# Optimization experiments

Measured on AMD Instinct MI355X. Metric: run time of the kernel, lower is better.

The kernel has to match this reference:

```python
import jax, jax.numpy as jnp
import numpy as np

IN_F = 256
OUT_F = 256
ALPHA = 0.2  # LeakyReLU negative slope


def _xavier(key, shape, gain=1.414):
    fan_in, fan_out = shape[0], shape[1]
    limit = gain * np.sqrt(6.0 / (fan_in + fan_out))
    return jax.random.uniform(key, shape, jnp.float32, -limit, limit)


def setup_inputs() -> dict:
    key = jax.random.key(0)
    k1, k2, k3, k4, k5, k6 = jax.random.split(key, 6)
    B, N = 8, 2048
    h = jax.random.normal(k1, (B, N, IN_F), jnp.float32)
    adj = jax.random.randint(k2, (B, N, N), 0, 2, jnp.int32)
    lrgt1 = jax.random.normal(k3, (B, N, OUT_F), jnp.float32)
    W1 = _xavier(k4, (IN_F, IN_F))
    W2 = _xavier(k5, (OUT_F, OUT_F))
    a = _xavier(k6, (2 * IN_F, 1))
    return {"h": h, "adj": adj, "lrgt1": lrgt1, "W1": W1, "W2": W2, "a": a}


def reference(h, adj, lrgt1, W1, W2, a):
    # Wh: [B,N,in], wlrgt: [B,N,out]
    Wh = jnp.matmul(h, W1)
    wlrgt = jnp.matmul(lrgt1, W2)
    # additive attention scores: e[b,i,j] = leaky_relu(Wh_i @ a1 + Wh_j @ a2)
    a1 = a[:IN_F, 0]   # [in]
    a2 = a[IN_F:, 0]   # [in]
    Wh1 = jnp.einsum('bnc,c->bn', Wh, a1)  # [B,N]
    Wh2 = jnp.einsum('bnc,c->bn', Wh, a2)  # [B,N]
    e = jax.nn.leaky_relu(Wh1[:, :, None] + Wh2[:, None, :], ALPHA)  # [B,N,N]
    neg = jnp.float32(-9e15)
    masked = jnp.where(adj > 0, e, neg)
    attention = jax.nn.softmax(masked, axis=2)
    # dropout p=0.0 / eval mode -> identity
    h_prime = jnp.matmul(attention, Wh)      # [B,N,in]
    gt_prime = jnp.matmul(attention, wlrgt)  # [B,N,out]
    return (jax.nn.elu(h_prime), jax.nn.elu(gt_prime))
```

## Files before the change

kernel.cpp:

```cpp
#include <hip/hip_runtime.h>
#include <hip/hip_bf16.h>

#define IN_F 256
#define NN   2048
#define BB   8

typedef unsigned short u16;
typedef __attribute__((ext_vector_type(8))) short short8x;
typedef __attribute__((ext_vector_type(4))) float float4x;

__device__ __forceinline__ u16 f2b(float f) {
    union { float f; unsigned int u; } x; x.f = f;
    unsigned int r = x.u + 0x7FFFu + ((x.u >> 16) & 1u);
    return (u16)(r >> 16);
}

__device__ __forceinline__ void transp_body(const float* __restrict__ src,
                                            u16* __restrict__ dst,
                                            int R, int C, int tid,
                                            float (*tile)[33])
{
    const int per = (R / 32) * (C / 32);
    const int b  = tid / per;
    const int tt = tid % per;
    const int jt = tt / (C / 32);
    const int ct = tt % (C / 32);
    src += (long)b * R * C;
    dst += (long)b * R * C;

    const int tx = threadIdx.x & 31, ty = threadIdx.x >> 5;
#pragma unroll
    for (int i = 0; i < 4; ++i)
        tile[ty + i * 8][tx] = src[(long)(jt * 32 + ty + i * 8) * C + ct * 32 + tx];
    __syncthreads();
#pragma unroll
    for (int i = 0; i < 4; ++i)
        dst[(long)(ct * 32 + ty + i * 8) * R + jt * 32 + tx] = f2b(tile[tx][ty + i * 8]);
}

__global__ __launch_bounds__(256) void prep(const float* __restrict__ h,
                                            const float* __restrict__ g,
                                            const float* __restrict__ W1,
                                            const float* __restrict__ W2,
                                            const float* __restrict__ a,
                                            u16* __restrict__ HbfT,
                                            u16* __restrict__ GbfT,
                                            u16* __restrict__ W1T,
                                            u16* __restrict__ W2T,
                                            float* __restrict__ v1,
                                            float* __restrict__ v2)
{
    __shared__ float tile[32][33];
    __shared__ float s1[IN_F], s2[IN_F];
    const int bid = blockIdx.x;

    if (bid < 4096) {
        transp_body(h, HbfT, NN, IN_F, bid, tile);
    } else if (bid < 8192) {
        transp_body(g, GbfT, NN, IN_F, bid - 4096, tile);
    } else if (bid < 8256) {
        transp_body(W1, W1T, IN_F, IN_F, bid - 8192, tile);
    } else if (bid < 8320) {
        transp_body(W2, W2T, IN_F, IN_F, bid - 8256, tile);
    } else {
        const int t = threadIdx.x;
        s1[t] = a[t];
        s2[t] = a[IN_F + t];
        __syncthreads();
        float acc1 = 0.f, acc2 = 0.f;
        for (int c = 0; c < IN_F; ++c) {
            float w = W1[t * IN_F + c];
            acc1 += w * s1[c];
            acc2 += w * s2[c];
        }
        v1[t] = acc1;
        v2[t] = acc2;
    }
}

__global__ __launch_bounds__(256) void rowdots(const float* __restrict__ h,
                                               const float* __restrict__ v1,
                                               const float* __restrict__ v2,
                                               float* __restrict__ Wh1,
                                               float* __restrict__ Wh2)
{
    const int wave = threadIdx.x >> 6;
    const int lane = threadIdx.x & 63;
    const long row = (long)blockIdx.x * 4 + wave;
    const int c0 = lane * 4;

    float4 v  = *(const float4*)(h + row * IN_F + c0);
    float4 a1 = *(const float4*)(v1 + c0);
    float4 a2 = *(const float4*)(v2 + c0);

    float s1 = v.x * a1.x + v.y * a1.y + v.z * a1.z + v.w * a1.w;
    float s2 = v.x * a2.x + v.y * a2.y + v.z * a2.z + v.w * a2.w;
#pragma unroll
    for (int off = 32; off; off >>= 1) {
        s1 += __shfl_xor(s1, off, 64);
        s2 += __shfl_xor(s2, off, 64);
    }
    if (lane == 0) { Wh1[row] = s1; Wh2[row] = s2; }
}

#define KSTEP(ksv, BC, BN_, AC, AN_, do_a, jnxt)                              \
    {                                                                         \
        if (do_a) {                                                           \
            _Pragma("unroll") for (int rt = 0; rt < 4; ++rt)                  \
                AN_[rt] = *(const short8x*)&ab[(((ksv) + 1) * 4 + rt) * 512 + lane * 8]; \
        }                                                                     \
        _Pragma("unroll") for (int ct = 0; ct < 4; ++ct)                      \
            BN_[ct] = *(const short8x*)(Bp + ct * 16 * NN + (jnxt));          \
        _Pragma("unroll") for (int rt = 0; rt < 4; ++rt)                      \
            _Pragma("unroll") for (int ct = 0; ct < 4; ++ct)                  \
                acc[rt][ct] = __builtin_amdgcn_mfma_f32_16x16x32_bf16(AC[rt], BC[ct], acc[rt][ct], 0, 0, 0); \
    }

#define CHUNK7(KCH, ADJC, ADJN)                                               \
    {                                                                         \
        const int j0 = (KCH) * 128;                                           \
        union { short8x v; u16 e[8]; } pk0, pk1, pk2, pk3;                    \
        _Pragma("unroll") for (int u = 0; u < 8; ++u) {                       \
            const float4 wv = *(const float4*)&wh2L[j0 + sg * 32 + u * 4];    \
            const float wf[4] = {wv.x, wv.y, wv.z, wv.w};                     \
            const int   av[4] = {ADJC[u].x, ADJC[u].y, ADJC[u].z, ADJC[u].w}; \
            _Pragma("unroll") for (int c = 0; c < 4; ++c) {                   \
                float x = wh1rr + wf[c];                                      \
                float ev = fmaxf(x, 0.2f * x);                                \
                float p = __expf(ev - mv);                                    \
                p = (av[c] > 0) ? p : 0.0f;                                   \
                lloc += p;                                                    \
                u16 fv = f2b(p);                                              \
                if (u < 2)      pk0.e[(u & 1) * 4 + c] = fv;                  \
                else if (u < 4) pk1.e[(u & 1) * 4 + c] = fv;                  \
                else if (u < 6) pk2.e[(u & 1) * 4 + c] = fv;                  \
                else            pk3.e[(u & 1) * 4 + c] = fv;                  \
            }                                                                 \
        }                                                                     \
        if ((KCH) < 15) {                                                     \
            const long o = adjR + ((KCH) + 1) * 128 + sg * 32;                \
            _Pragma("unroll") for (int u = 0; u < 8; ++u)                     \
                ADJN[u] = *(const int4*)(adj + o + u * 4);                    \
        }                                                                     \
        u16* ab = &Afrag[(KCH) & 1][0];                                       \
        *(short8x*)&ab[wbase0]       = pk0.v;                                 \
        *(short8x*)&ab[wbase0 + 128] = pk1.v;                                 \
        *(short8x*)&ab[wbase0 + 256] = pk2.v;                                 \
        *(short8x*)&ab[wbase0 + 384] = pk3.v;                                 \
        asm volatile("s_waitcnt lgkmcnt(0)\n\ts_barrier" ::: "memory");       \
        _Pragma("unroll") for (int rt = 0; rt < 4; ++rt)                      \
            A0[rt] = *(const short8x*)&ab[rt * 512 + lane * 8];               \
        KSTEP(0, B0, B1, A0, A1, 1, j0 + 1 * 32 + bq8)                        \
        KSTEP(1, B1, B0, A1, A0, 1, j0 + 2 * 32 + bq8)                        \
        KSTEP(2, B0, B1, A0, A1, 1, j0 + 3 * 32 + bq8)                        \
        KSTEP(3, B1, B0, A1, A0, 0, (((KCH) < 15) ? (j0 + 128) : j0) + bq8)   \
    }

__global__ __launch_bounds__(256, 2) void attn_mfma(
    const int* __restrict__ adj,
    const u16* __restrict__ HbfT, const u16* __restrict__ GbfT,
    const float* __restrict__ Wh1, const float* __restrict__ Wh2,
    u16* __restrict__ PH, u16* __restrict__ PG)
{
    const int t = threadIdx.x;
    const int wave = t >> 6, lane = t & 63;
    const int b   = blockIdx.x & 7;
    const int idx = blockIdx.x >> 3;
    const int mat = idx & 1;
    const int rbl = idx >> 1;
    const long gi0 = ((long)b * 32 + rbl) * 64;

    __shared__ __align__(16) u16 Afrag[2][8192];
    __shared__ float wh2L[2048];
    __shared__ float sred[256];
    __shared__ float ssc[65];

    const int rr = t >> 2, sg = t & 3;
    const long adjR = (gi0 + rr) * (long)NN;
    const float* wh2b = Wh2 + (long)b * NN;
    const float wh1rr = Wh1[gi0 + rr];

    {
        float4 w0 = *(const float4*)(wh2b + t * 8);
        float4 w1 = *(const float4*)(wh2b + t * 8 + 4);
        *(float4*)&wh2L[t * 8]     = w0;
        *(float4*)&wh2L[t * 8 + 4] = w1;
        float m = fmaxf(fmaxf(fmaxf(w0.x, w0.y), fmaxf(w0.z, w0.w)),
                        fmaxf(fmaxf(w1.x, w1.y), fmaxf(w1.z, w1.w)));
        sred[t] = m;
    }
    __syncthreads();
    if (t < 64) {
        float v = fmaxf(fmaxf(sred[t * 4], sred[t * 4 + 1]),
                        fmaxf(sred[t * 4 + 2], sred[t * 4 + 3]));
#pragma unroll
        for (int off = 32; off; off >>= 1) v = fmaxf(v, __shfl_xor(v, off, 64));
        if (t == 0) ssc[64] = v;
    }
    __syncthreads();
    const float mm = wh1rr + ssc[64];
    const float mv = (mm >= 0.f) ? mm : 0.2f * mm;

    const int wbase0 = (sg * 4 + (rr >> 4)) * 512 + (rr & 15) * 8;

    float4x acc[4][4];
#pragma unroll
    for (int rt = 0; rt < 4; ++rt)
#pragma unroll
        for (int ct = 0; ct < 4; ++ct) acc[rt][ct] = (float4x)0.0f;

    const int bn = lane & 15, bq = lane >> 4, bq8 = bq * 8;
    const u16* Bp = (mat ? GbfT : HbfT) + (long)b * IN_F * NN
                  + (long)(wave * 64 + bn) * NN;

    float lloc = 0.f;

    short8x A0[4], A1[4], B0[4], B1[4];
    int4 adjA[8], adjB[8];

#pragma unroll
    for (int u = 0; u < 8; ++u)
        adjA[u] = *(const int4*)(adj + adjR + sg * 32 + u * 4);
#pragma unroll
    for (int u = 0; u < 8; ++u)
        adjB[u] = *(const int4*)(adj + adjR + 128 + sg * 32 + u * 4);
#pragma unroll
    for (int ct = 0; ct < 4; ++ct)
        B0[ct] = *(const short8x*)(Bp + ct * 16 * NN + bq8);

    for (int kp = 0; kp < 8; ++kp) {
        CHUNK7(kp * 2,     adjA, adjB)
        CHUNK7(kp * 2 + 1, adjB, adjA)
    }

    sred[t] = lloc;
    __syncthreads();
    if (t < 64) {
        float v = sred[t * 4] + sred[t * 4 + 1] + sred[t * 4 + 2] + sred[t * 4 + 3];
        ssc[t] = 1.0f / v;
    }
    __syncthreads();

    u16* dst = mat ? PG : PH;
    const int colb = wave * 64;
#pragma unroll
    for (int rt = 0; rt < 4; ++rt)
#pragma unroll
        for (int ct = 0; ct < 4; ++ct) {
            const int c = colb + ct * 16 + bn;
#pragma unroll
            for (int reg = 0; reg < 4; ++reg) {
                const int rl = rt * 16 + bq * 4 + reg;
                const float il = ssc[rl];
                const long row = gi0 + rl;
                dst[row * IN_F + c] = f2b(acc[rt][ct][reg] * il);
            }
        }
}

__global__ __launch_bounds__(256) void epi2(const u16* __restrict__ PH,
                                            const u16* __restrict__ PG,
                                            const u16* __restrict__ W1T,
                                            const u16* __restrict__ W2T,
                                            float* __restrict__ out)
{
    int bid = blockIdx.x;
    const u16* X;
    const u16* WT;
    float* o;
    if (bid < 512) { X = PH; WT = W1T; o = out; }
    else           { X = PG; WT = W2T; o = out + (long)BB * NN * IN_F; bid -= 512; }

    const int t = threadIdx.x;
    const int wave = t >> 6, lane = t & 63;
    const long i0 = (long)bid * 32;

    __shared__ __align__(16) u16 Afrag[8 * 2 * 64 * 8];

    const int m = t >> 3, ks0 = t & 7, rt0 = m >> 4, lm = m & 15;
    const u16* xp = X + (i0 + m) * IN_F + ks0 * 32;
#pragma unroll
    for (int q = 0; q < 4; ++q) {
        short8x v = *(const short8x*)(xp + q * 8);
        *(short8x*)&Afrag[((ks0 * 2 + rt0) * 64 + lm + q * 16) * 8] = v;
    }
    __syncthreads();

    float4x acc[2][4];
#pragma unroll
    for (int rt = 0; rt < 2; ++rt)
#pragma unroll
        for (int ct = 0; ct < 4; ++ct) acc[rt][ct] = (float4x)0.0f;

    const int bn = lane & 15, bq = lane >> 4;
#pragma unroll
    for (int ks = 0; ks < 8; ++ks) {
        short8x A0 = *(const short8x*)&Afrag[((ks * 2 + 0) * 64 + lane) * 8];
        short8x A1 = *(const short8x*)&Afrag[((ks * 2 + 1) * 64 + lane) * 8];
#pragma unroll
        for (int ct = 0; ct < 4; ++ct) {
            const int n = wave * 64 + ct * 16 + bn;
            short8x Bw = *(const short8x*)(WT + n * IN_F + ks * 32 + bq * 8);
            acc[0][ct] = __builtin_amdgcn_mfma_f32_16x16x32_bf16(A0, Bw, acc[0][ct], 0, 0, 0);
            acc[1][ct] = __builtin_amdgcn_mfma_f32_16x16x32_bf16(A1, Bw, acc[1][ct], 0, 0, 0);
        }
    }

#pragma unroll
    for (int rt = 0; rt < 2; ++rt)
#pragma unroll
        for (int ct = 0; ct < 4; ++ct) {
            const int n = wave * 64 + ct * 16 + bn;
#pragma unroll
            for (int reg = 0; reg < 4; ++reg) {
                const long row = i0 + rt * 16 + bq * 4 + reg;
                float v = acc[rt][ct][reg];
                v = (v > 0.f) ? v : (__expf(v) - 1.f);
                o[row * IN_F + n] = v;
            }
        }
}

extern "C" void kernel_launch(void* const* d_in, const int* in_sizes, int n_in,
                              void* d_out, int out_size, void* d_ws, size_t ws_size,
                              hipStream_t stream)
{
    int ih = -1, ig = -1, iadj = -1, iw1 = -1, iw2 = -1, ia = -1;
    for (int i = 0; i < n_in; ++i) {
        int s = in_sizes[i];
        if      (s == BB * NN * NN)   { if (iadj < 0) iadj = i; }
        else if (s == BB * NN * IN_F) { if (ih < 0) ih = i; else if (ig < 0) ig = i; }
        else if (s == IN_F * IN_F)    { if (iw1 < 0) iw1 = i; else if (iw2 < 0) iw2 = i; }
        else if (s == 2 * IN_F)       { if (ia < 0) ia = i; }
    }
    if (ih < 0 || ig < 0 || iadj < 0 || iw1 < 0 || iw2 < 0 || ia < 0) {
        ih = 0; iadj = 1; ig = 2; iw1 = 3; iw2 = 4; ia = 5;
    }
    const float* h     = (const float*)d_in[ih];
    const int*   adj   = (const int*)  d_in[iadj];
    const float* lrgt1 = (const float*)d_in[ig];
    const float* W1    = (const float*)d_in[iw1];
    const float* W2    = (const float*)d_in[iw2];
    const float* a     = (const float*)d_in[ia];
    float* out = (float*)d_out;

    float* ws   = (float*)d_ws;
    float* v1   = ws;
    float* v2   = v1 + IN_F;
    float* Wh1  = v2 + IN_F;
    float* Wh2  = Wh1 + BB * NN;
    u16* W1T  = (u16*)(Wh2 + BB * NN);
    u16* W2T  = W1T + IN_F * IN_F;
    u16* HbfT = W2T + IN_F * IN_F;
    u16* GbfT = HbfT + (long)BB * IN_F * NN;
    u16* PH   = GbfT + (long)BB * IN_F * NN;
    u16* PG   = PH + (long)BB * NN * IN_F;

    const int nrows = BB * NN;

    prep     <<<8321,        256, 0, stream>>>(h, lrgt1, W1, W2, a,
                                               HbfT, GbfT, W1T, W2T, v1, v2);
    rowdots  <<<nrows / 4,   256, 0, stream>>>(h, v1, v2, Wh1, Wh2);
    attn_mfma<<<nrows / 32,  256, 0, stream>>>(adj, HbfT, GbfT, Wh1, Wh2, PH, PG);
    epi2     <<<2 * nrows / 32, 256, 0, stream>>>(PH, PG, W1T, W2T, out);
}
```

Baseline: 324.1 us.

## Halve attention row tile to 32 rows, bit-pack adjacency mask, vectorize transpose

The attention kernel now processes 32 query rows per block instead of 64, with 8 threads per row and half the accumulator tiles, so register and LDS use drop and launch bounds rise to 4 blocks per SM. The grid doubles. Adjacency values for the next chunk are loaded as four int4 values and packed into a 16-bit mask, which replaces holding 16 int4 registers. The prep transpose now uses float4 loads and ushort4 stores. The aim is higher occupancy and fewer registers, at the cost of rereading the B (HbfT/GbfT) operand twice as often across blocks.

```diff
diff --git a/kernel.cpp b/kernel.cpp
--- a/kernel.cpp
+++ b/kernel.cpp
@@ -15,10 +15,10 @@
     return (u16)(r >> 16);
 }
 
-__device__ __forceinline__ void transp_body(const float* __restrict__ src,
-                                            u16* __restrict__ dst,
-                                            int R, int C, int tid,
-                                            float (*tile)[33])
+__device__ __forceinline__ void transp_body4(const float* __restrict__ src,
+                                             u16* __restrict__ dst,
+                                             int R, int C, int tid,
+                                             float (*tile)[33])
 {
     const int per = (R / 32) * (C / 32);
     const int b  = tid / per;
@@ -28,14 +28,21 @@
     src += (long)b * R * C;
     dst += (long)b * R * C;
 
-    const int tx = threadIdx.x & 31, ty = threadIdx.x >> 5;
-#pragma unroll
-    for (int i = 0; i < 4; ++i)
-        tile[ty + i * 8][tx] = src[(long)(jt * 32 + ty + i * 8) * C + ct * 32 + tx];
-    __syncthreads();
-#pragma unroll
-    for (int i = 0; i < 4; ++i)
-        dst[(long)(ct * 32 + ty + i * 8) * R + jt * 32 + tx] = f2b(tile[tx][ty + i * 8]);
+    const int t = threadIdx.x;
+    const int lr = t >> 3, lc = (t & 7) * 4;
+    float4 v = *(const float4*)(src + (long)(jt * 32 + lr) * C + ct * 32 + lc);
+    tile[lr][lc + 0] = v.x;
+    tile[lr][lc + 1] = v.y;
+    tile[lr][lc + 2] = v.z;
+    tile[lr][lc + 3] = v.w;
+    __syncthreads();
+    const int c = t >> 3, r4 = (t & 7) * 4;
+    ushort4 o;
+    o.x = f2b(tile[r4 + 0][c]);
+    o.y = f2b(tile[r4 + 1][c]);
+    o.z = f2b(tile[r4 + 2][c]);
+    o.w = f2b(tile[r4 + 3][c]);
+    *(ushort4*)(dst + (long)(ct * 32 + c) * R + jt * 32 + r4) = o;
 }
 
 __global__ __launch_bounds__(256) void prep(const float* __restrict__ h,
@@ -55,13 +62,13 @@
     const int bid = blockIdx.x;
 
     if (bid < 4096) {
-        transp_body(h, HbfT, NN, IN_F, bid, tile);
+        transp_body4(h, HbfT, NN, IN_F, bid, tile);
     } else if (bid < 8192) {
-        transp_body(g, GbfT, NN, IN_F, bid - 4096, tile);
+        transp_body4(g, GbfT, NN, IN_F, bid - 4096, tile);
     } else if (bid < 8256) {
-        transp_body(W1, W1T, IN_F, IN_F, bid - 8192, tile);
+        transp_body4(W1, W1T, IN_F, IN_F, bid - 8192, tile);
     } else if (bid < 8320) {
-        transp_body(W2, W2T, IN_F, IN_F, bid - 8256, tile);
+        transp_body4(W2, W2T, IN_F, IN_F, bid - 8256, tile);
     } else {
         const int t = threadIdx.x;
         s1[t] = a[t];
@@ -103,60 +110,63 @@
     if (lane == 0) { Wh1[row] = s1; Wh2[row] = s2; }
 }
 
-#define KSTEP(ksv, BC, BN_, AC, AN_, do_a, jnxt)                              \
+#define KS8(KSV, BC, BN_, jnxt)                                               \
     {                                                                         \
-        if (do_a) {                                                           \
-            _Pragma("unroll") for (int rt = 0; rt < 4; ++rt)                  \
-                AN_[rt] = *(const short8x*)&ab[(((ksv) + 1) * 4 + rt) * 512 + lane * 8]; \
-        }                                                                     \
+        short8x Ar0 = *(const short8x*)&ab[(((KSV) * 2 + 0) * 64 + lane) * 8];\
+        short8x Ar1 = *(const short8x*)&ab[(((KSV) * 2 + 1) * 64 + lane) * 8];\
         _Pragma("unroll") for (int ct = 0; ct < 4; ++ct)                      \
             BN_[ct] = *(const short8x*)(Bp + ct * 16 * NN + (jnxt));          \
-        _Pragma("unroll") for (int rt = 0; rt < 4; ++rt)                      \
-            _Pragma("unroll") for (int ct = 0; ct < 4; ++ct)                  \
-                acc[rt][ct] = __builtin_amdgcn_mfma_f32_16x16x32_bf16(AC[rt], BC[ct], acc[rt][ct], 0, 0, 0); \
-    }
-
-#define CHUNK7(KCH, ADJC, ADJN)                                               \
+        _Pragma("unroll") for (int ct = 0; ct < 4; ++ct) {                    \
+            acc[0][ct] = __builtin_amdgcn_mfma_f32_16x16x32_bf16(Ar0, BC[ct], acc[0][ct], 0, 0, 0); \
+            acc[1][ct] = __builtin_amdgcn_mfma_f32_16x16x32_bf16(Ar1, BC[ct], acc[1][ct], 0, 0, 0); \
+        }                                                                     \
+    }
+
+#define PK4(I4, BASE)                                                         \
+    pb |= ((unsigned)(I4.x > 0) << (BASE))     | ((unsigned)(I4.y > 0) << ((BASE)+1)) | \
+          ((unsigned)(I4.z > 0) << ((BASE)+2)) | ((unsigned)(I4.w > 0) << ((BASE)+3));
+
+#define CHUNK8(KCH)                                                           \
     {                                                                         \
         const int j0 = (KCH) * 128;                                           \
-        union { short8x v; u16 e[8]; } pk0, pk1, pk2, pk3;                    \
-        _Pragma("unroll") for (int u = 0; u < 8; ++u) {                       \
-            const float4 wv = *(const float4*)&wh2L[j0 + sg * 32 + u * 4];    \
+        union { short8x v; u16 e[8]; } pk0, pk1;                              \
+        _Pragma("unroll") for (int u = 0; u < 4; ++u) {                       \
+            const float4 wv = *(const float4*)&wh2L[j0 + sg * 16 + u * 4];    \
             const float wf[4] = {wv.x, wv.y, wv.z, wv.w};                     \
-            const int   av[4] = {ADJC[u].x, ADJC[u].y, ADJC[u].z, ADJC[u].w}; \
             _Pragma("unroll") for (int c = 0; c < 4; ++c) {                   \
                 float x = wh1rr + wf[c];                                      \
                 float ev = fmaxf(x, 0.2f * x);                                \
                 float p = __expf(ev - mv);                                    \
-                p = (av[c] > 0) ? p : 0.0f;                                   \
+                p = ((mk >> (u * 4 + c)) & 1u) ? p : 0.0f;                    \
                 lloc += p;                                                    \
                 u16 fv = f2b(p);                                              \
-                if (u < 2)      pk0.e[(u & 1) * 4 + c] = fv;                  \
-                else if (u < 4) pk1.e[(u & 1) * 4 + c] = fv;                  \
-                else if (u < 6) pk2.e[(u & 1) * 4 + c] = fv;                  \
-                else            pk3.e[(u & 1) * 4 + c] = fv;                  \
+                if (u < 2) pk0.e[u * 4 + c] = fv;                             \
+                else       pk1.e[(u - 2) * 4 + c] = fv;                       \
             }                                                                 \
         }                                                                     \
         if ((KCH) < 15) {                                                     \
-            const long o = adjR + ((KCH) + 1) * 128 + sg * 32;                \
-            _Pragma("unroll") for (int u = 0; u < 8; ++u)                     \
-                ADJN[u] = *(const int4*)(adj + o + u * 4);                    \
+            const long o = adjR + ((KCH) + 1) * 128 + sg * 16;                \
+            i0 = *(const int4*)(adj + o);                                     \
+            i1 = *(const int4*)(adj + o + 4);                                 \
+            i2 = *(const int4*)(adj + o + 8);                                 \
+            i3 = *(const int4*)(adj + o + 12);                                \
         }                                                                     \
         u16* ab = &Afrag[(KCH) & 1][0];                                       \
         *(short8x*)&ab[wbase0]       = pk0.v;                                 \
         *(short8x*)&ab[wbase0 + 128] = pk1.v;                                 \
-        *(short8x*)&ab[wbase0 + 256] = pk2.v;                                 \
-        *(short8x*)&ab[wbase0 + 384] = pk3.v;                                 \
         asm volatile("s_waitcnt lgkmcnt(0)\n\ts_barrier" ::: "memory");       \
-        _Pragma("unroll") for (int rt = 0; rt < 4; ++rt)                      \
-            A0[rt] = *(const short8x*)&ab[rt * 512 + lane * 8];               \
-        KSTEP(0, B0, B1, A0, A1, 1, j0 + 1 * 32 + bq8)                        \
-        KSTEP(1, B1, B0, A1, A0, 1, j0 + 2 * 32 + bq8)                        \
-        KSTEP(2, B0, B1, A0, A1, 1, j0 + 3 * 32 + bq8)                        \
-        KSTEP(3, B1, B0, A1, A0, 0, (((KCH) < 15) ? (j0 + 128) : j0) + bq8)   \
-    }
-
-__global__ __launch_bounds__(256, 2) void attn_mfma(
+        KS8(0, B0, B1, j0 + 1 * 32 + bq8)                                     \
+        KS8(1, B1, B0, j0 + 2 * 32 + bq8)                                     \
+        KS8(2, B0, B1, j0 + 3 * 32 + bq8)                                     \
+        KS8(3, B1, B0, (((KCH) < 15) ? (j0 + 128) : j0) + bq8)                \
+        if ((KCH) < 15) {                                                     \
+            unsigned pb = 0;                                                  \
+            PK4(i0, 0) PK4(i1, 4) PK4(i2, 8) PK4(i3, 12)                      \
+            mk = pb;                                                          \
+        }                                                                     \
+    }
+
+__global__ __launch_bounds__(256, 4) void attn_mfma(
     const int* __restrict__ adj,
     const u16* __restrict__ HbfT, const u16* __restrict__ GbfT,
     const float* __restrict__ Wh1, const float* __restrict__ Wh2,
@@ -168,14 +178,14 @@
     const int idx = blockIdx.x >> 3;
     const int mat = idx & 1;
     const int rbl = idx >> 1;
-    const long gi0 = ((long)b * 32 + rbl) * 64;
-
-    __shared__ __align__(16) u16 Afrag[2][8192];
+    const long gi0 = ((long)b * 64 + rbl) * 32;
+
+    __shared__ __align__(16) u16 Afrag[2][4096];
     __shared__ float wh2L[2048];
     __shared__ float sred[256];
-    __shared__ float ssc[65];
-
-    const int rr = t >> 2, sg = t & 3;
+    __shared__ float ssc[33];
+
+    const int rr = t >> 3, sg = t & 7;
     const long adjR = (gi0 + rr) * (long)NN;
     const float* wh2b = Wh2 + (long)b * NN;
     const float wh1rr = Wh1[gi0 + rr];
@@ -195,17 +205,18 @@
                         fmaxf(sred[t * 4 + 2], sred[t * 4 + 3]));
 #pragma unroll
         for (int off = 32; off; off >>= 1) v = fmaxf(v, __shfl_xor(v, off, 64));
-        if (t == 0) ssc[64] = v;
-    }
-    __syncthreads();
-    const float mm = wh1rr + ssc[64];
+        if (t == 0) ssc[32] = v;
+    }
+    __syncthreads();
+    const float mm = wh1rr + ssc[32];
     const float mv = (mm >= 0.f) ? mm : 0.2f * mm;
 
-    const int wbase0 = (sg * 4 + (rr >> 4)) * 512 + (rr & 15) * 8;
-
-    float4x acc[4][4];
-#pragma unroll
-    for (int rt = 0; rt < 4; ++rt)
+    const int wbase0 = ((sg >> 1) * 2 + (rr >> 4)) * 512
+                     + ((rr & 15) + 32 * (sg & 1)) * 8;
+
+    float4x acc[2][4];
+#pragma unroll
+    for (int rt = 0; rt < 2; ++rt)
 #pragma unroll
         for (int ct = 0; ct < 4; ++ct) acc[rt][ct] = (float4x)0.0f;
 
@@ -214,29 +225,34 @@
                   + (long)(wave * 64 + bn) * NN;
 
     float lloc = 0.f;
-
-    short8x A0[4], A1[4], B0[4], B1[4];
-    int4 adjA[8], adjB[8];
-
-#pragma unroll
-    for (int u = 0; u < 8; ++u)
-        adjA[u] = *(const int4*)(adj + adjR + sg * 32 + u * 4);
-#pragma unroll
-    for (int u = 0; u < 8; ++u)
-        adjB[u] = *(const int4*)(adj + adjR + 128 + sg * 32 + u * 4);
+    unsigned mk = 0;
+    int4 i0, i1, i2, i3;
+    short8x B0[4], B1[4];
+
+    i0 = *(const int4*)(adj + adjR + sg * 16);
+    i1 = *(const int4*)(adj + adjR + sg * 16 + 4);
+    i2 = *(const int4*)(adj + adjR + sg * 16 + 8);
+    i3 = *(const int4*)(adj + adjR + sg * 16 + 12);
+    {
+        unsigned pb = 0;
+        PK4(i0, 0) PK4(i1, 4) PK4(i2, 8) PK4(i3, 12)
+        mk = pb;
+    }
 #pragma unroll
     for (int ct = 0; ct < 4; ++ct)
         B0[ct] = *(const short8x*)(Bp + ct * 16 * NN + bq8);
 
     for (int kp = 0; kp < 8; ++kp) {
-        CHUNK7(kp * 2,     adjA, adjB)
-        CHUNK7(kp * 2 + 1, adjB, adjA)
+        CHUNK8(kp * 2)
+        CHUNK8(kp * 2 + 1)
     }
 
     sred[t] = lloc;
     __syncthreads();
-    if (t < 64) {
-        float v = sred[t * 4] + sred[t * 4 + 1] + sred[t * 4 + 2] + sred[t * 4 + 3];
+    if (t < 32) {
+        float v = sred[t * 8];
+#pragma unroll
+        for (int k = 1; k < 8; ++k) v += sred[t * 8 + k];
         ssc[t] = 1.0f / v;
     }
     __syncthreads();
@@ -244,7 +260,7 @@
     u16* dst = mat ? PG : PH;
     const int colb = wave * 64;
 #pragma unroll
-    for (int rt = 0; rt < 4; ++rt)
+    for (int rt = 0; rt < 2; ++rt)
 #pragma unroll
         for (int ct = 0; ct < 4; ++ct) {
             const int c = colb + ct * 16 + bn;
@@ -361,6 +377,6 @@
     prep     <<<8321,        256, 0, stream>>>(h, lrgt1, W1, W2, a,
                                                HbfT, GbfT, W1T, W2T, v1, v2);
     rowdots  <<<nrows / 4,   256, 0, stream>>>(h, v1, v2, Wh1, Wh2);
-    attn_mfma<<<nrows / 32,  256, 0, stream>>>(adj, HbfT, GbfT, Wh1, Wh2, PH, PG);
+    attn_mfma<<<2 * nrows / 32, 256, 0, stream>>>(adj, HbfT, GbfT, Wh1, Wh2, PH, PG);
     epi2     <<<2 * nrows / 32, 256, 0, stream>>>(PH, PG, W1T, W2T, out);
 }
```

New measurement: 381.2 us. 1.18x slower.
